# Performance work log

Hardware: AMD Instinct MI355X
Metric: run time of the kernel (lower is better)

The kernel has to match this reference:

```python
import jax, jax.numpy as jnp
import numpy as np
from math import sqrt, exp

EMBED_DIM = 1024
HEAD_DIM = 128
LAMBDA_INIT = 0.8 - 0.6 * exp(-0.3 * 0)  # layer_index = 0


def setup_inputs() -> dict:
    key = jax.random.key(0)
    ks = jax.random.split(key, 12)
    B, Tq, Tk = 4, 2048, 2048
    s = 1.0 / sqrt(EMBED_DIM)
    return {
        "x": jax.random.normal(ks[0], (B, Tq, EMBED_DIM), jnp.float32),
        "encoder_out": jax.random.normal(ks[1], (B, Tk, EMBED_DIM), jnp.float32),
        "W_q": jax.random.normal(ks[2], (EMBED_DIM, HEAD_DIM), jnp.float32) * s,
        "b_q": jnp.zeros((HEAD_DIM,), jnp.float32),
        "W_k": jax.random.normal(ks[3], (EMBED_DIM, HEAD_DIM), jnp.float32) * s,
        "b_k": jnp.zeros((HEAD_DIM,), jnp.float32),
        "W_v": jax.random.normal(ks[4], (EMBED_DIM, HEAD_DIM), jnp.float32) * s,
        "b_v": jnp.zeros((HEAD_DIM,), jnp.float32),
        "lambda_q1": jax.random.normal(ks[5], (HEAD_DIM,), jnp.float32) * 0.1,
        "lambda_k1": jax.random.normal(ks[6], (HEAD_DIM,), jnp.float32) * 0.1,
        "lambda_q2": jax.random.normal(ks[7], (HEAD_DIM,), jnp.float32) * 0.1,
        "lambda_k2": jax.random.normal(ks[8], (HEAD_DIM,), jnp.float32) * 0.1,
        "lambda_init": jnp.asarray(LAMBDA_INIT, jnp.float32),
    }


def reference(x, encoder_out, W_q, b_q, W_k, b_k, W_v, b_v,
              lambda_q1, lambda_k1, lambda_q2, lambda_k2, lambda_init):
    # scalar learned lambda
    lam = jnp.exp(lambda_q1 @ lambda_k1) - jnp.exp(lambda_q2 @ lambda_k2) + lambda_init
    q = x @ W_q + b_q                      # [B, Tq, D]
    k = encoder_out @ W_k + b_k            # [B, Tk, D]
    v = encoder_out @ W_v + b_v            # [B, Tk, D]
    d = HEAD_DIM // 2
    q1, q2 = q[..., :d], q[..., d:]
    k1, k2 = k[..., :d], k[..., d:]
    scale = 1.0 / sqrt(d)
    s1 = jnp.einsum("bqd,bkd->bqk", q1, k1) * scale
    s2 = jnp.einsum("bqd,bkd->bqk", q2, k2) * scale
    w = jax.nn.softmax(s1, axis=-1) - lam * jax.nn.softmax(s2, axis=-1)
    return jnp.einsum("bqk,bkd->bqd", w, v)   # [B, Tq, D]
```

## Files before the change

kernel.cpp:

```cpp
#include <hip/hip_runtime.h>
#include <hip/hip_bf16.h>


#define TQ 2048
#define TK 2048
#define EMB 1024
#define HD 128
#define MQ 8192

typedef __attribute__((ext_vector_type(8))) short short8;
typedef __attribute__((ext_vector_type(4))) float floatx4;

__device__ __forceinline__ unsigned short f2bf(float f) {
  union { float f; unsigned u; } v; v.f = f;
  unsigned r = v.u + 0x7fffu + ((v.u >> 16) & 1u);
  return (unsigned short)(r >> 16);
}
__device__ __forceinline__ float bf2f(unsigned short s) {
  union { unsigned u; float f; } v; v.u = ((unsigned)s) << 16;
  return v.f;
}

typedef const __attribute__((address_space(1))) unsigned int guint;
typedef __attribute__((address_space(3))) unsigned int luint;
__device__ __forceinline__ void gl16(const void* g, void* l) {
  __builtin_amdgcn_global_load_lds((guint*)g, (luint*)l, 16, 0, 0);
}

__global__ __launch_bounds__(256) void cvtWT_kernel(
    const float* __restrict__ Wq, const float* __restrict__ Wk,
    const float* __restrict__ Wv, unsigned short* __restrict__ WqT,
    unsigned short* __restrict__ WkT, unsigned short* __restrict__ WvT,
    const float* __restrict__ lq1, const float* __restrict__ lk1,
    const float* __restrict__ lq2, const float* __restrict__ lk2,
    const float* __restrict__ linit, float* __restrict__ lam_out) {
  const int g = blockIdx.y;
  if (g == 3) {
    if (blockIdx.x == 0 && threadIdx.x < 64) {
      int j = threadIdx.x;
      float s1 = lq1[j] * lk1[j] + lq1[j + 64] * lk1[j + 64];
      float s2 = lq2[j] * lk2[j] + lq2[j + 64] * lk2[j + 64];
      for (int off = 1; off < 64; off <<= 1) {
        s1 += __shfl_xor(s1, off);
        s2 += __shfl_xor(s2, off);
      }
      if (j == 0) lam_out[0] = __expf(s1) - __expf(s2) + linit[0];
    }
    return;
  }
  const float* W = (g == 0) ? Wq : (g == 1) ? Wk : Wv;
  unsigned short* WT = (g == 0) ? WqT : (g == 1) ? WkT : WvT;
  int idx = blockIdx.x * 256 + threadIdx.x;
  int n = idx >> 10, k = idx & 1023;
  WT[idx] = f2bf(W[(size_t)k * HD + n]);
}

__global__ __launch_bounds__(256) void gemm_proj_kernel(
    const float* __restrict__ x, const float* __restrict__ enc,
    const unsigned short* __restrict__ WqT, const unsigned short* __restrict__ WkT,
    const unsigned short* __restrict__ WvT,
    const float* __restrict__ bq, const float* __restrict__ bk,
    const float* __restrict__ bv,
    unsigned short* __restrict__ qb, unsigned short* __restrict__ kb,
    unsigned short* __restrict__ vbT) {
  __shared__ __align__(16) float Ab[2][32 * 64];
  __shared__ __align__(16) unsigned short Bb[2][128 * 64];
  const int t = threadIdx.x;
  const int w = t >> 6, lane = t & 63;
  const int lo = lane & 15, quad = lane >> 4;
  const int wm = w & 1, wn = w >> 1;
  const int g = blockIdx.y;
  const size_t m0 = (size_t)blockIdx.x * 32;
  const float* A = (g == 0) ? x : enc;
  const unsigned short* BT = (g == 0) ? WqT : (g == 1) ? WkT : WvT;
  const float* bias = (g == 0) ? bq : (g == 1) ? bk : bv;

  const float* gA[2];
  int ldsAoff[2];
#pragma unroll
  for (int j = 0; j < 2; ++j) {
    int c = 2 * w + j;
    int row = 4 * c + (lane >> 4);
    int colb = ((lane & 15) * 16) ^ ((row & 7) << 4);
    gA[j] = A + (m0 + row) * EMB + (colb >> 2);
    ldsAoff[j] = c * 1024;
  }
  const unsigned short* gB[4];
  int ldsBoff[4];
#pragma unroll
  for (int j = 0; j < 4; ++j) {
    int c = 4 * w + j;
    int row = 8 * c + (lane >> 3);
    int colb = ((lane & 7) * 16) ^ ((row & 7) << 4);
    gB[j] = BT + (size_t)row * EMB + (colb >> 1);
    ldsBoff[j] = c * 1024;
  }

  floatx4 acc[4];
  const floatx4 zz = {0.f, 0.f, 0.f, 0.f};
#pragma unroll
  for (int i = 0; i < 4; ++i) acc[i] = zz;

  const int xr = (lo & 7) << 4;

  auto stage = [&](int kt, int bsel) {
#pragma unroll
    for (int j = 0; j < 2; ++j) gl16(gA[j] + kt, (char*)&Ab[bsel][0] + ldsAoff[j]);
#pragma unroll
    for (int j = 0; j < 4; ++j) gl16(gB[j] + kt, (char*)&Bb[bsel][0] + ldsBoff[j]);
  };

  auto compute = [&](int bsel) {
    const char* Arow = (const char*)&Ab[bsel][(16 * wm + lo) * 64];
    const char* Bbase = (const char*)&Bb[bsel][0];
#pragma unroll
    for (int ks = 0; ks < 2; ++ks) {
      int a0 = (ks * 128 + quad * 32) ^ xr;
      float4 fa = *(const float4*)(Arow + a0);
      float4 fb = *(const float4*)(Arow + (a0 ^ 16));
      short8 af;
      af[0] = (short)f2bf(fa.x); af[1] = (short)f2bf(fa.y);
      af[2] = (short)f2bf(fa.z); af[3] = (short)f2bf(fa.w);
      af[4] = (short)f2bf(fb.x); af[5] = (short)f2bf(fb.y);
      af[6] = (short)f2bf(fb.z); af[7] = (short)f2bf(fb.w);
      int b0 = (ks * 64 + quad * 16) ^ xr;
#pragma unroll
      for (int nt = 0; nt < 4; ++nt) {
        int row = wn * 64 + nt * 16 + lo;
        short8 bfr = *(const short8*)(Bbase + row * 128 + b0);
        acc[nt] = __builtin_amdgcn_mfma_f32_16x16x32_bf16(af, bfr, acc[nt], 0, 0, 0);
      }
    }
  };

  stage(0, 0);
  __syncthreads();

  for (int kt = 0; kt < EMB; kt += 128) {
    stage(kt + 64, 1);
    compute(0);
    __syncthreads();
    if (kt + 128 < EMB) stage(kt + 128, 0);
    compute(1);
    __syncthreads();
  }

  const int mrow = 16 * wm + quad * 4;
  if (g < 2) {
    unsigned short* Y = (g == 0) ? qb : kb;
    const float sc = (g == 0) ? 0.125f : 1.0f;
#pragma unroll
    for (int nt = 0; nt < 4; ++nt) {
      float bn = bias[wn * 64 + nt * 16 + lo];
#pragma unroll
      for (int r = 0; r < 4; ++r)
        Y[(m0 + mrow + r) * HD + wn * 64 + nt * 16 + lo] = f2bf((acc[nt][r] + bn) * sc);
    }
  } else {
#pragma unroll
    for (int nt = 0; nt < 4; ++nt) {
      float bn = bias[wn * 64 + nt * 16 + lo];
      unsigned long long pk = 0;
#pragma unroll
      for (int r = 0; r < 4; ++r)
        pk |= (unsigned long long)f2bf(acc[nt][r] + bn) << (16 * r);
      *(unsigned long long*)&vbT[(size_t)(wn * 64 + nt * 16 + lo) * MQ + m0 + mrow] = pk;
    }
  }
}

__global__ __launch_bounds__(512, 4) void attn_split_kernel(
    const unsigned short* __restrict__ qb, const unsigned short* __restrict__ kb,
    const unsigned short* __restrict__ vbT,
    unsigned short* __restrict__ pO1, unsigned short* __restrict__ pO2,
    float2* __restrict__ pstats, int nkeys) {
  __shared__ __align__(16) unsigned short Kls[64][136];
  __shared__ __align__(16) unsigned short Vt[128][72];
  __shared__ __align__(16) unsigned short Pls[8][16][72];

  const int t = threadIdx.x;
  const int w = t >> 6;
  const int g = w >> 2;
  const int wv = w & 3;
  const int lane = t & 63;
  const int lo = lane & 15;
  const int quad = lane >> 4;
  const int q8 = quad * 8;
  const int b = blockIdx.y;
  const int q0 = blockIdx.x * 64;
  const int ksp = blockIdx.z;
  const int kt0 = ksp * nkeys;
  const int ksTot = TK / nkeys;
  const size_t kbase = (size_t)b * TK;

  const size_t qrow = (size_t)b * TQ + q0 + wv * 16 + lo;
  short8 qf[2];
#pragma unroll
  for (int ks = 0; ks < 2; ++ks)
    qf[ks] = *(const short8*)&qb[qrow * HD + g * 64 + ks * 32 + q8];

  floatx4 o[8];
  const floatx4 zz = {0.f, 0.f, 0.f, 0.f};
#pragma unroll
  for (int i = 0; i < 8; ++i) o[i] = zz;
  float m[4], l[4];
#pragma unroll
  for (int r = 0; r < 4; ++r) { m[r] = -1e30f; l[r] = 0.f; }

  for (int kt = kt0; kt < kt0 + nkeys; kt += 64) {
#pragma unroll
    for (int i = 0; i < 2; ++i) {
      int c = t + 512 * i;
      int key = c >> 4, f0 = (c & 15) * 8;
      *(int4*)&Kls[key][f0] =
          *(const int4*)&kb[(kbase + kt + key) * HD + f0];
      int f = c >> 3, k0 = (c & 7) * 8;
      *(int4*)&Vt[f][k0] =
          *(const int4*)&vbT[(size_t)f * MQ + kbase + kt + k0];
    }
    __syncthreads();

    floatx4 s[4];
#pragma unroll
    for (int i = 0; i < 4; ++i) s[i] = zz;
#pragma unroll
    for (int ks = 0; ks < 2; ++ks)
#pragma unroll
      for (int nt = 0; nt < 4; ++nt) {
        short8 kf = *(const short8*)&Kls[nt * 16 + lo][g * 64 + ks * 32 + q8];
        s[nt] = __builtin_amdgcn_mfma_f32_16x16x32_bf16(qf[ks], kf, s[nt], 0, 0, 0);
      }

    float tm[4];
#pragma unroll
    for (int r = 0; r < 4; ++r) {
      float a = fmaxf(fmaxf(s[0][r], s[1][r]), fmaxf(s[2][r], s[3][r]));
#pragma unroll
      for (int oo = 1; oo < 16; oo <<= 1) a = fmaxf(a, __shfl_xor(a, oo));
      tm[r] = a;
    }
    bool grow = false;
#pragma unroll
    for (int r = 0; r < 4; ++r) grow = grow || (tm[r] > m[r] + 5.f);
    if (__any(grow)) {
#pragma unroll
      for (int r = 0; r < 4; ++r) {
        float mn = fmaxf(m[r], tm[r]);
        float al = __expf(m[r] - mn);
        m[r] = mn;
        l[r] *= al;
#pragma unroll
        for (int nt = 0; nt < 8; ++nt) o[nt][r] *= al;
      }
    }
#pragma unroll
    for (int r = 0; r < 4; ++r) {
      float ls = 0.f;
#pragma unroll
      for (int nt = 0; nt < 4; ++nt) {
        float p = __expf(s[nt][r] - m[r]);
        ls += p;
        Pls[w][quad * 4 + r][nt * 16 + lo] = f2bf(p);
      }
#pragma unroll
      for (int oo = 1; oo < 16; oo <<= 1) ls += __shfl_xor(ls, oo);
      l[r] += ls;
    }

#pragma unroll
    for (int ks = 0; ks < 2; ++ks) {
      short8 p8 = *(const short8*)&Pls[w][lo][ks * 32 + q8];
#pragma unroll
      for (int nt = 0; nt < 8; ++nt) {
        short8 vf = *(const short8*)&Vt[nt * 16 + lo][ks * 32 + q8];
        o[nt] = __builtin_amdgcn_mfma_f32_16x16x32_bf16(p8, vf, o[nt], 0, 0, 0);
      }
    }
    __syncthreads();
  }

  unsigned short* Y = g ? pO2 : pO1;
#pragma unroll
  for (int r = 0; r < 4; ++r) {
    int rowb = q0 + wv * 16 + quad * 4 + r;
    size_t idx = ((size_t)(ksp * 4 + b)) * TQ + rowb;
    if (lo == 0)
      pstats[((size_t)(g * ksTot + ksp) * 4 + b) * TQ + rowb] = make_float2(m[r], l[r]);
#pragma unroll
    for (int nt = 0; nt < 8; ++nt)
      Y[idx * HD + nt * 16 + lo] = f2bf(o[nt][r]);
  }
}

__global__ __launch_bounds__(256) void attn_combine_kernel(
    const unsigned short* __restrict__ pO1, const unsigned short* __restrict__ pO2,
    const float2* __restrict__ pstats, const float* __restrict__ lam_ptr,
    float* __restrict__ out, int ksn) {
  const int t = threadIdx.x;
  const int b = blockIdx.y;
  const int row = blockIdx.x * 16 + (t >> 4);
  const int dg = t & 15;

  float m1s[8], l1s[8], m2s[8], l2s[8];
  float M1 = -1e30f, M2 = -1e30f;
  for (int s = 0; s < ksn; ++s) {
    float2 fa = pstats[((size_t)(s) * 4 + b) * TQ + row];
    float2 fb = pstats[((size_t)(ksn + s) * 4 + b) * TQ + row];
    m1s[s] = fa.x; l1s[s] = fa.y; m2s[s] = fb.x; l2s[s] = fb.y;
    M1 = fmaxf(M1, fa.x); M2 = fmaxf(M2, fb.x);
  }
  float L1 = 0.f, L2 = 0.f, e1[8], e2[8];
  for (int s = 0; s < ksn; ++s) {
    e1[s] = __expf(m1s[s] - M1); e2[s] = __expf(m2s[s] - M2);
    L1 += l1s[s] * e1[s]; L2 += l2s[s] * e2[s];
  }
  float a1[8], a2[8];
#pragma unroll
  for (int j = 0; j < 8; ++j) { a1[j] = 0.f; a2[j] = 0.f; }
  for (int s = 0; s < ksn; ++s) {
    size_t base = (((size_t)(s * 4 + b)) * TQ + row) * HD + dg * 8;
    int4 r1 = *(const int4*)&pO1[base];
    int4 r2 = *(const int4*)&pO2[base];
    const unsigned short* u1 = (const unsigned short*)&r1;
    const unsigned short* u2 = (const unsigned short*)&r2;
#pragma unroll
    for (int j = 0; j < 8; ++j) {
      a1[j] += bf2f(u1[j]) * e1[s];
      a2[j] += bf2f(u2[j]) * e2[s];
    }
  }
  const float i1 = 1.f / L1;
  const float i2 = lam_ptr[0] / L2;
  float4* op = (float4*)&out[((size_t)b * TQ + row) * HD + dg * 8];
  op[0] = make_float4(a1[0] * i1 - a2[0] * i2, a1[1] * i1 - a2[1] * i2,
                      a1[2] * i1 - a2[2] * i2, a1[3] * i1 - a2[3] * i2);
  op[1] = make_float4(a1[4] * i1 - a2[4] * i2, a1[5] * i1 - a2[5] * i2,
                      a1[6] * i1 - a2[6] * i2, a1[7] * i1 - a2[7] * i2);
}

extern "C" void kernel_launch(void* const* d_in, const int* in_sizes, int n_in,
                              void* d_out, int out_size, void* d_ws, size_t ws_size,
                              hipStream_t stream) {
  const float* x    = (const float*)d_in[0];
  const float* enc  = (const float*)d_in[1];
  const float* Wq   = (const float*)d_in[2];
  const float* bq   = (const float*)d_in[3];
  const float* Wk   = (const float*)d_in[4];
  const float* bk   = (const float*)d_in[5];
  const float* Wv   = (const float*)d_in[6];
  const float* bv   = (const float*)d_in[7];
  const float* lq1  = (const float*)d_in[8];
  const float* lk1  = (const float*)d_in[9];
  const float* lq2  = (const float*)d_in[10];
  const float* lk2  = (const float*)d_in[11];
  const float* lini = (const float*)d_in[12];
  float* out = (float*)d_out;

  char* p = (char*)d_ws;
  float* lam = (float*)p;                       p += 256;
  unsigned short* qb  = (unsigned short*)p;     p += (size_t)MQ * HD * 2;
  unsigned short* kb  = (unsigned short*)p;     p += (size_t)MQ * HD * 2;
  unsigned short* vbT = (unsigned short*)p;     p += (size_t)MQ * HD * 2;
  unsigned short* WqT = (unsigned short*)p;     p += (size_t)EMB * HD * 2;
  unsigned short* WkT = (unsigned short*)p;     p += (size_t)EMB * HD * 2;
  unsigned short* WvT = (unsigned short*)p;     p += (size_t)EMB * HD * 2;
  const size_t base_need = (size_t)(p - (char*)d_ws);

  const size_t per_ks = (size_t)4 * TQ * 16 + 2ull * 4 * TQ * HD * 2;
  int KS = 4;
  while (KS > 1 && base_need + (size_t)KS * per_ks > ws_size) KS >>= 1;

  float2* pstats = (float2*)p;                  p += (size_t)KS * 4 * TQ * 16;
  unsigned short* pO1 = (unsigned short*)p;     p += (size_t)KS * 4 * TQ * HD * 2;
  unsigned short* pO2 = (unsigned short*)p;

  hipLaunchKernelGGL(cvtWT_kernel, dim3(512, 4), dim3(256), 0, stream,
                     Wq, Wk, Wv, WqT, WkT, WvT, lq1, lk1, lq2, lk2, lini, lam);
  hipLaunchKernelGGL(gemm_proj_kernel, dim3(MQ / 32, 3), dim3(256), 0, stream,
                     x, enc, WqT, WkT, WvT, bq, bk, bv, qb, kb, vbT);
  hipLaunchKernelGGL(attn_split_kernel, dim3(TQ / 64, 4, KS), dim3(512), 0, stream,
                     qb, kb, vbT, pO1, pO2, pstats, TK / KS);
  hipLaunchKernelGGL(attn_combine_kernel, dim3(TQ / 16, 4), dim3(256), 0, stream,
                     pO1, pO2, pstats, lam, out, KS);
}
```

Baseline: 178.4 us.

## Swizzle attention LDS tiles, defer row reductions, and raise key-split count

Drops the padded shared-memory arrays for K, V-transposed and P in favour of unpadded tiles with an XOR swizzle on the 16-byte column index, so MFMA operand reads avoid bank conflicts while using less LDS. The per-tile row-max shuffle now runs only inside the rare rescale branch, and the row-sum shuffle is moved out of the key loop to a single reduction at the end. The key-split factor rises from 4 to 8, giving more blocks at the cost of more partial outputs for the combine kernel to read and merge. The rescale check now uses per-lane maxima, so lanes within a row may see different m values when a rescale does not fire. That needs care for correctness.

```diff
diff --git a/kernel.cpp b/kernel.cpp
--- a/kernel.cpp
+++ b/kernel.cpp
@@ -174,9 +174,9 @@
     const unsigned short* __restrict__ vbT,
     unsigned short* __restrict__ pO1, unsigned short* __restrict__ pO2,
     float2* __restrict__ pstats, int nkeys) {
-  __shared__ __align__(16) unsigned short Kls[64][136];
-  __shared__ __align__(16) unsigned short Vt[128][72];
-  __shared__ __align__(16) unsigned short Pls[8][16][72];
+  __shared__ __align__(16) unsigned short Kls[64 * 128];
+  __shared__ __align__(16) unsigned short Vt[128 * 64];
+  __shared__ __align__(16) unsigned short Pls[8][16 * 64];
 
   const int t = threadIdx.x;
   const int w = t >> 6;
@@ -186,6 +186,7 @@
   const int lo = lane & 15;
   const int quad = lane >> 4;
   const int q8 = quad * 8;
+  const int xsw = (lo & 7) << 4;
   const int b = blockIdx.y;
   const int q0 = blockIdx.x * 64;
   const int ksp = blockIdx.z;
@@ -211,12 +212,14 @@
 #pragma unroll
     for (int i = 0; i < 2; ++i) {
       int c = t + 512 * i;
-      int key = c >> 4, f0 = (c & 15) * 8;
-      *(int4*)&Kls[key][f0] =
-          *(const int4*)&kb[(kbase + kt + key) * HD + f0];
-      int f = c >> 3, k0 = (c & 7) * 8;
-      *(int4*)&Vt[f][k0] =
-          *(const int4*)&vbT[(size_t)f * MQ + kbase + kt + k0];
+      int key = c >> 4;
+      int kByte = key * 256 + ((((c & 15) * 16)) ^ ((key & 7) << 4));
+      *(int4*)((char*)Kls + kByte) =
+          *(const int4*)&kb[(kbase + kt + key) * HD + (c & 15) * 8];
+      int f = c >> 3;
+      int vByte = f * 128 + ((((c & 7) * 16)) ^ ((f & 7) << 4));
+      *(int4*)((char*)Vt + vByte) =
+          *(const int4*)&vbT[(size_t)f * MQ + kbase + kt + (c & 7) * 8];
     }
     __syncthreads();
 
@@ -227,25 +230,26 @@
     for (int ks = 0; ks < 2; ++ks)
 #pragma unroll
       for (int nt = 0; nt < 4; ++nt) {
-        short8 kf = *(const short8*)&Kls[nt * 16 + lo][g * 64 + ks * 32 + q8];
+        int row = nt * 16 + lo;
+        short8 kf = *(const short8*)((const char*)Kls + row * 256 +
+                                     ((g * 128 + ks * 64 + quad * 16) ^ xsw));
         s[nt] = __builtin_amdgcn_mfma_f32_16x16x32_bf16(qf[ks], kf, s[nt], 0, 0, 0);
       }
 
-    float tm[4];
-#pragma unroll
-    for (int r = 0; r < 4; ++r) {
-      float a = fmaxf(fmaxf(s[0][r], s[1][r]), fmaxf(s[2][r], s[3][r]));
-#pragma unroll
-      for (int oo = 1; oo < 16; oo <<= 1) a = fmaxf(a, __shfl_xor(a, oo));
-      tm[r] = a;
-    }
+    float a4[4];
+#pragma unroll
+    for (int r = 0; r < 4; ++r)
+      a4[r] = fmaxf(fmaxf(s[0][r], s[1][r]), fmaxf(s[2][r], s[3][r]));
     bool grow = false;
 #pragma unroll
-    for (int r = 0; r < 4; ++r) grow = grow || (tm[r] > m[r] + 5.f);
+    for (int r = 0; r < 4; ++r) grow = grow || (a4[r] > m[r] + 5.f);
     if (__any(grow)) {
 #pragma unroll
       for (int r = 0; r < 4; ++r) {
-        float mn = fmaxf(m[r], tm[r]);
+        float tm = a4[r];
+#pragma unroll
+        for (int oo = 1; oo < 16; oo <<= 1) tm = fmaxf(tm, __shfl_xor(tm, oo));
+        float mn = fmaxf(m[r], tm);
         float al = __expf(m[r] - mn);
         m[r] = mn;
         l[r] *= al;
@@ -255,29 +259,36 @@
     }
 #pragma unroll
     for (int r = 0; r < 4; ++r) {
+      int rr = quad * 4 + r;
+      int rsw = (rr & 7) << 4;
       float ls = 0.f;
 #pragma unroll
       for (int nt = 0; nt < 4; ++nt) {
         float p = __expf(s[nt][r] - m[r]);
         ls += p;
-        Pls[w][quad * 4 + r][nt * 16 + lo] = f2bf(p);
-      }
-#pragma unroll
-      for (int oo = 1; oo < 16; oo <<= 1) ls += __shfl_xor(ls, oo);
+        *(unsigned short*)((char*)Pls[w] + rr * 128 + (((nt * 16 + lo) * 2) ^ rsw)) =
+            f2bf(p);
+      }
       l[r] += ls;
     }
 
 #pragma unroll
     for (int ks = 0; ks < 2; ++ks) {
-      short8 p8 = *(const short8*)&Pls[w][lo][ks * 32 + q8];
+      int cb = (ks * 64 + quad * 16);
+      short8 p8 = *(const short8*)((const char*)Pls[w] + lo * 128 + (cb ^ xsw));
 #pragma unroll
       for (int nt = 0; nt < 8; ++nt) {
-        short8 vf = *(const short8*)&Vt[nt * 16 + lo][ks * 32 + q8];
+        short8 vf = *(const short8*)((const char*)Vt + (nt * 16 + lo) * 128 + (cb ^ xsw));
         o[nt] = __builtin_amdgcn_mfma_f32_16x16x32_bf16(p8, vf, o[nt], 0, 0, 0);
       }
     }
     __syncthreads();
   }
+
+#pragma unroll
+  for (int r = 0; r < 4; ++r)
+#pragma unroll
+    for (int oo = 1; oo < 16; oo <<= 1) l[r] += __shfl_xor(l[r], oo);
 
   unsigned short* Y = g ? pO2 : pO1;
 #pragma unroll
@@ -367,7 +378,7 @@
   const size_t base_need = (size_t)(p - (char*)d_ws);
 
   const size_t per_ks = (size_t)4 * TQ * 16 + 2ull * 4 * TQ * HD * 2;
-  int KS = 4;
+  int KS = 8;
   while (KS > 1 && base_need + (size_t)KS * per_ks > ws_size) KS >>= 1;
 
   float2* pstats = (float2*)p;                  p += (size_t)KS * 4 * TQ * 16;
```

Result: no change. 177.8 us (-0.4%).
